# Kernel tuning notes

Measured on AMD Instinct MI355X. Metric: run time of the kernel, lower is better.

The kernel has to match this reference:

```python
import jax, jax.numpy as jnp
import numpy as np

DIM = 1024
RANK = 16


def setup_inputs() -> dict:
    key = jax.random.key(0)
    ks = jax.random.split(key, 9)
    s = 0.02
    return {
        "x": jax.random.normal(ks[0], (2, 4096, DIM), dtype=jnp.float32),
        "W_qkv": jax.random.normal(ks[1], (3 * DIM, DIM), dtype=jnp.float32) * s,
        "b_qkv": jax.random.normal(ks[2], (3 * DIM,), dtype=jnp.float32) * s,
        "A_q": jax.random.normal(ks[3], (RANK, DIM), dtype=jnp.float32) * s,
        "B_q": jax.random.normal(ks[4], (DIM, RANK), dtype=jnp.float32) * s,
        "A_k": jax.random.normal(ks[5], (RANK, DIM), dtype=jnp.float32) * s,
        "B_k": jax.random.normal(ks[6], (DIM, RANK), dtype=jnp.float32) * s,
        "A_v": jax.random.normal(ks[7], (RANK, DIM), dtype=jnp.float32) * s,
        "B_v": jax.random.normal(ks[8], (DIM, RANK), dtype=jnp.float32) * s,
        "alpha": jnp.float32(0.5),
    }


def reference(x, W_qkv, b_qkv, A_q, B_q, A_k, B_k, A_v, B_v, alpha):
    # base fused QKV projection: [B, S, 3*dim]
    qkv = jnp.einsum("bsd,od->bso", x, W_qkv) + b_qkv
    # low-rank adapters: x @ A.T @ B.T, rank=16
    lora_q = jnp.einsum("bsr,dr->bsd", jnp.einsum("bsd,rd->bsr", x, A_q), B_q)
    lora_k = jnp.einsum("bsr,dr->bsd", jnp.einsum("bsd,rd->bsr", x, A_k), B_k)
    lora_v = jnp.einsum("bsr,dr->bsd", jnp.einsum("bsd,rd->bsr", x, A_v), B_v)
    # scaled add into q/k/v slices (concat order matches torch slice layout)
    delta = jnp.concatenate([lora_q, lora_k, lora_v], axis=-1)
    return qkv + alpha * delta
```

## Files before the change

### kernel.cpp

```cpp
#include <hip/hip_runtime.h>
#include <stdint.h>

#define DIM    1024
#define RANK   16
#define M_TOT  8192
#define N_TOT  3072
#define K_TOT  1024

#define BM 256
#define BN 128
#define BK 64
#define NT (K_TOT / BK)

typedef __attribute__((ext_vector_type(8))) short  s8v;
typedef __attribute__((ext_vector_type(4))) float  f4v;

__device__ __forceinline__ unsigned short f2bf(float f) {
    union { float f; unsigned int u; } v; v.f = f;
    unsigned int u = v.u;
    u += 0x7FFFu + ((u >> 16) & 1u);
    return (unsigned short)(u >> 16);
}

__device__ __forceinline__ void gload_lds16(const unsigned short* g,
                                            unsigned short* l) {
    __builtin_amdgcn_global_load_lds(
        (const __attribute__((address_space(1))) void*)g,
        (__attribute__((address_space(3))) void*)l,
        16, 0, 0);
}

__global__ __launch_bounds__(256)
void prep(const float4* __restrict__ x, ushort4* __restrict__ xb,
          const float* __restrict__ W,
          const float* __restrict__ Aq, const float* __restrict__ Bq,
          const float* __restrict__ Ak, const float* __restrict__ Bk,
          const float* __restrict__ Av, const float* __restrict__ Bv,
          const float* __restrict__ alpha_p,
          unsigned short* __restrict__ Wb) {
    const int tid = threadIdx.x;
    if (blockIdx.x < 2048) {
        int i = blockIdx.x * 256 + tid;
        #pragma unroll
        for (int k = 0; k < 4; ++k) {
            float4 v = x[i];
            ushort4 o;
            o.x = f2bf(v.x); o.y = f2bf(v.y); o.z = f2bf(v.z); o.w = f2bf(v.w);
            xb[i] = o;
            i += 2048 * 256;
        }
    } else {
        const int bid2 = blockIdx.x - 2048;
        const int sel  = bid2 >> 6;
        const int rb   = bid2 & 63;
        const float* Am = (sel == 0) ? Aq : (sel == 1) ? Ak : Av;
        const float* Bm = (sel == 0) ? Bq : (sel == 1) ? Bk : Bv;

        __shared__ float sb[16][RANK];
        {
            const int row = rb * 16 + (tid >> 4);
            sb[tid >> 4][tid & 15] = alpha_p[0] * Bm[row * RANK + (tid & 15)];
        }
        __syncthreads();

        float4 a4[RANK];
        #pragma unroll
        for (int r = 0; r < RANK; ++r)
            a4[r] = ((const float4*)(Am + r * DIM))[tid];

        #pragma unroll
        for (int row = 0; row < 16; ++row) {
            const int o = sel * 1024 + rb * 16 + row;
            float4 w = ((const float4*)(W + (size_t)o * DIM))[tid];
            #pragma unroll
            for (int r = 0; r < RANK; ++r) {
                const float s = sb[row][r];
                w.x += s * a4[r].x; w.y += s * a4[r].y;
                w.z += s * a4[r].z; w.w += s * a4[r].w;
            }
            ushort4 ov;
            ov.x = f2bf(w.x); ov.y = f2bf(w.y); ov.z = f2bf(w.z); ov.w = f2bf(w.w);
            ((ushort4*)(Wb + (size_t)o * DIM))[tid] = ov;
        }
    }
}

__global__ __launch_bounds__(512, 2)
void gemm_bt(const unsigned short* __restrict__ Xb,
             const unsigned short* __restrict__ Wb,
             const float* __restrict__ bias,
             float* __restrict__ out) {
    __shared__ __align__(16) unsigned short As[3][BM * BK];
    __shared__ __align__(16) unsigned short Bs[3][BN * BK];

    const int tid  = threadIdx.x;
    const int wave = tid >> 6;
    const int lane = tid & 63;
    const int l15  = lane & 15;
    const int lq   = lane >> 4;
    const int wr   = wave >> 1;
    const int wc   = wave & 1;

    const int bid = blockIdx.x;
    const int xcd = bid & 7;
    const int s   = bid >> 3;
    const int bn  = s % 24;
    const int bm  = xcd * 4 + s / 24;

    const unsigned short* aptr[4];
    const unsigned short* bptr[2];
    int aoff[4], boff[2];
    #pragma unroll
    for (int u = 0; u < 4; ++u) {
        const int c   = wave * 4 + u;
        const int row = ((c >> 1) << 4) + l15;
        const int col = ((c & 1) << 5) + (lq << 3);
        aptr[u] = Xb + (size_t)(bm * BM + row) * K_TOT + col;
        aoff[u] = c * 512;
    }
    #pragma unroll
    for (int u = 0; u < 2; ++u) {
        const int c   = wave * 2 + u;
        const int row = ((c >> 1) << 4) + l15;
        const int col = ((c & 1) << 5) + (lq << 3);
        bptr[u] = Wb + (size_t)(bn * BN + row) * K_TOT + col;
        boff[u] = c * 512;
    }

    #pragma unroll
    for (int t = 0; t < 2; ++t) {
        #pragma unroll
        for (int u = 0; u < 4; ++u) gload_lds16(aptr[u] + t * BK, &As[t][aoff[u]]);
        #pragma unroll
        for (int u = 0; u < 2; ++u) gload_lds16(bptr[u] + t * BK, &Bs[t][boff[u]]);
    }
    asm volatile("s_waitcnt vmcnt(6)" ::: "memory");
    __builtin_amdgcn_sched_barrier(0);
    __builtin_amdgcn_s_barrier();
    __builtin_amdgcn_sched_barrier(0);

    f4v acc[4][4] = {};

    #pragma unroll 1
    for (int q = 0; q < NT; ++q) {
        const int r    = q % 3;
        const int r2   = (q + 2) % 3;
        const int kg   = (q + 2) * BK;
        const bool iss = (q + 2) < NT;
        const s8v* Avp = (const s8v*)As[r];
        const s8v* Bvp = (const s8v*)Bs[r];

        {
            s8v af[4], bf[4];
            #pragma unroll
            for (int i = 0; i < 4; ++i) {
                af[i] = Avp[((wr * 4 + i) * 2 + 0) * 64 + lane];
                bf[i] = Bvp[((wc * 4 + i) * 2 + 0) * 64 + lane];
            }
            if (iss) {
                gload_lds16(aptr[0] + kg, &As[r2][aoff[0]]);
                gload_lds16(aptr[1] + kg, &As[r2][aoff[1]]);
                gload_lds16(bptr[0] + kg, &Bs[r2][boff[0]]);
            }
            __builtin_amdgcn_sched_barrier(0);
            __builtin_amdgcn_s_barrier();
            asm volatile("s_waitcnt lgkmcnt(0)" ::: "memory");
            __builtin_amdgcn_sched_barrier(0);
            __builtin_amdgcn_s_setprio(1);
            #pragma unroll
            for (int i = 0; i < 4; ++i)
                #pragma unroll
                for (int j = 0; j < 4; ++j)
                    acc[i][j] = __builtin_amdgcn_mfma_f32_16x16x32_bf16(
                        af[i], bf[j], acc[i][j], 0, 0, 0);
            __builtin_amdgcn_s_setprio(0);
            __builtin_amdgcn_sched_barrier(0);
            __builtin_amdgcn_s_barrier();
            __builtin_amdgcn_sched_barrier(0);
        }

        {
            s8v af[4], bf[4];
            #pragma unroll
            for (int i = 0; i < 4; ++i) {
                af[i] = Avp[((wr * 4 + i) * 2 + 1) * 64 + lane];
                bf[i] = Bvp[((wc * 4 + i) * 2 + 1) * 64 + lane];
            }
            if (iss) {
                gload_lds16(aptr[2] + kg, &As[r2][aoff[2]]);
                gload_lds16(aptr[3] + kg, &As[r2][aoff[3]]);
                gload_lds16(bptr[1] + kg, &Bs[r2][boff[1]]);
            }
            __builtin_amdgcn_sched_barrier(0);
            __builtin_amdgcn_s_barrier();
            asm volatile("s_waitcnt lgkmcnt(0)" ::: "memory");
            __builtin_amdgcn_sched_barrier(0);
            __builtin_amdgcn_s_setprio(1);
            #pragma unroll
            for (int i = 0; i < 4; ++i)
                #pragma unroll
                for (int j = 0; j < 4; ++j)
                    acc[i][j] = __builtin_amdgcn_mfma_f32_16x16x32_bf16(
                        af[i], bf[j], acc[i][j], 0, 0, 0);
            __builtin_amdgcn_s_setprio(0);
            __builtin_amdgcn_sched_barrier(0);
            if (q < NT - 2) {
                asm volatile("s_waitcnt vmcnt(6)" ::: "memory");
            } else if (q == NT - 2) {
                asm volatile("s_waitcnt vmcnt(0)" ::: "memory");
            }
            __builtin_amdgcn_sched_barrier(0);
            __builtin_amdgcn_s_barrier();
            __builtin_amdgcn_sched_barrier(0);
        }
    }

    const int col_base = bn * BN + wc * 64;
    const int row_base = bm * BM + wr * 64 + lq * 4;
    #pragma unroll
    for (int j = 0; j < 4; ++j) {
        const int col = col_base + j * 16 + l15;
        const float bv = bias[col];
        #pragma unroll
        for (int i = 0; i < 4; ++i) {
            const int row = row_base + i * 16;
            #pragma unroll
            for (int r = 0; r < 4; ++r)
                out[(size_t)(row + r) * N_TOT + col] = acc[i][j][r] + bv;
        }
    }
}

extern "C" void kernel_launch(void* const* d_in, const int* in_sizes, int n_in,
                              void* d_out, int out_size, void* d_ws, size_t ws_size,
                              hipStream_t stream) {
    const float* x     = (const float*)d_in[0];
    const float* W     = (const float*)d_in[1];
    const float* b     = (const float*)d_in[2];
    const float* Aq    = (const float*)d_in[3];
    const float* Bq    = (const float*)d_in[4];
    const float* Ak    = (const float*)d_in[5];
    const float* Bk    = (const float*)d_in[6];
    const float* Av    = (const float*)d_in[7];
    const float* Bv    = (const float*)d_in[8];
    const float* alpha = (const float*)d_in[9];
    float* out = (float*)d_out;

    unsigned short* xb = (unsigned short*)d_ws;
    unsigned short* Wb = (unsigned short*)((char*)d_ws + (size_t)M_TOT * K_TOT * 2);

    prep<<<2048 + 192, 256, 0, stream>>>((const float4*)x, (ushort4*)xb,
                                         W, Aq, Bq, Ak, Bk, Av, Bv, alpha, Wb);

    gemm_bt<<<(M_TOT / BM) * (N_TOT / BN), 512, 0, stream>>>(xb, Wb, b, out);
}
```

Baseline: 233.4 us.

## Retile block order into 4x8 groups, fully unroll K loop, trim barriers

```diff
diff --git a/kernel.cpp b/kernel.cpp
--- a/kernel.cpp
+++ b/kernel.cpp
@@ -101,11 +101,13 @@
     const int wr   = wave >> 1;
     const int wc   = wave & 1;
 
-    const int bid = blockIdx.x;
-    const int xcd = bid & 7;
-    const int s   = bid >> 3;
-    const int bn  = s % 24;
-    const int bm  = xcd * 4 + s / 24;
+    const int bid   = blockIdx.x;
+    const int xcd   = bid & 7;
+    const int s     = bid >> 3;
+    const int chunk = s >> 5;
+    const int t5    = s & 31;
+    const int bm    = xcd * 4 + (t5 >> 3);
+    const int bn    = chunk * 8 + (t5 & 7);
 
     const unsigned short* aptr[4];
     const unsigned short* bptr[2];
@@ -141,28 +143,35 @@
 
     f4v acc[4][4] = {};
 
-    #pragma unroll 1
+    #pragma unroll
     for (int q = 0; q < NT; ++q) {
         const int r    = q % 3;
         const int r2   = (q + 2) % 3;
         const int kg   = (q + 2) * BK;
         const bool iss = (q + 2) < NT;
+
         const s8v* Avp = (const s8v*)As[r];
         const s8v* Bvp = (const s8v*)Bs[r];
 
-        {
+        #pragma unroll
+        for (int t = 0; t < 2; ++t) {
             s8v af[4], bf[4];
             #pragma unroll
             for (int i = 0; i < 4; ++i) {
-                af[i] = Avp[((wr * 4 + i) * 2 + 0) * 64 + lane];
-                bf[i] = Bvp[((wc * 4 + i) * 2 + 0) * 64 + lane];
+                af[i] = Avp[((wr * 4 + i) * 2 + t) * 64 + lane];
+                bf[i] = Bvp[((wc * 4 + i) * 2 + t) * 64 + lane];
             }
             if (iss) {
-                gload_lds16(aptr[0] + kg, &As[r2][aoff[0]]);
-                gload_lds16(aptr[1] + kg, &As[r2][aoff[1]]);
-                gload_lds16(bptr[0] + kg, &Bs[r2][boff[0]]);
-            }
-            __builtin_amdgcn_sched_barrier(0);
+                if (t == 0) {
+                    gload_lds16(aptr[0] + kg, &As[r2][aoff[0]]);
+                    gload_lds16(aptr[1] + kg, &As[r2][aoff[1]]);
+                    gload_lds16(bptr[0] + kg, &Bs[r2][boff[0]]);
+                } else {
+                    gload_lds16(aptr[2] + kg, &As[r2][aoff[2]]);
+                    gload_lds16(aptr[3] + kg, &As[r2][aoff[3]]);
+                    gload_lds16(bptr[1] + kg, &Bs[r2][boff[1]]);
+                }
+            }
             __builtin_amdgcn_s_barrier();
             asm volatile("s_waitcnt lgkmcnt(0)" ::: "memory");
             __builtin_amdgcn_sched_barrier(0);
@@ -174,44 +183,20 @@
                     acc[i][j] = __builtin_amdgcn_mfma_f32_16x16x32_bf16(
                         af[i], bf[j], acc[i][j], 0, 0, 0);
             __builtin_amdgcn_s_setprio(0);
-            __builtin_amdgcn_sched_barrier(0);
-            __builtin_amdgcn_s_barrier();
-            __builtin_amdgcn_sched_barrier(0);
-        }
-
-        {
-            s8v af[4], bf[4];
-            #pragma unroll
-            for (int i = 0; i < 4; ++i) {
-                af[i] = Avp[((wr * 4 + i) * 2 + 1) * 64 + lane];
-                bf[i] = Bvp[((wc * 4 + i) * 2 + 1) * 64 + lane];
-            }
-            if (iss) {
-                gload_lds16(aptr[2] + kg, &As[r2][aoff[2]]);
-                gload_lds16(aptr[3] + kg, &As[r2][aoff[3]]);
-                gload_lds16(bptr[1] + kg, &Bs[r2][boff[1]]);
-            }
-            __builtin_amdgcn_sched_barrier(0);
-            __builtin_amdgcn_s_barrier();
-            asm volatile("s_waitcnt lgkmcnt(0)" ::: "memory");
-            __builtin_amdgcn_sched_barrier(0);
-            __builtin_amdgcn_s_setprio(1);
-            #pragma unroll
-            for (int i = 0; i < 4; ++i)
-                #pragma unroll
-                for (int j = 0; j < 4; ++j)
-                    acc[i][j] = __builtin_amdgcn_mfma_f32_16x16x32_bf16(
-                        af[i], bf[j], acc[i][j], 0, 0, 0);
-            __builtin_amdgcn_s_setprio(0);
-            __builtin_amdgcn_sched_barrier(0);
-            if (q < NT - 2) {
-                asm volatile("s_waitcnt vmcnt(6)" ::: "memory");
-            } else if (q == NT - 2) {
-                asm volatile("s_waitcnt vmcnt(0)" ::: "memory");
-            }
-            __builtin_amdgcn_sched_barrier(0);
-            __builtin_amdgcn_s_barrier();
-            __builtin_amdgcn_sched_barrier(0);
+
+            if (t == 0) {
+                __builtin_amdgcn_s_barrier();
+            } else {
+                if (q < NT - 2)
+                    asm volatile("s_waitcnt vmcnt(6)" ::: "memory");
+                else if (q == NT - 2)
+                    asm volatile("s_waitcnt vmcnt(0)" ::: "memory");
+                if (q < NT - 1) {
+                    __builtin_amdgcn_sched_barrier(0);
+                    __builtin_amdgcn_s_barrier();
+                    __builtin_amdgcn_sched_barrier(0);
+                }
+            }
         }
     }
 
```

Result: slower. 245.6 us (+5.2%).
